# Optimization experiments

Hardware: AMD Instinct MI355X
Metric: run time of the kernel (lower is better)

Reference implementation:

```python
import jax, jax.numpy as jnp
import numpy as np

B, C, H, W = 4, 256, 64, 64
CI = 128  # inter_channels = in_channels // 2
EPS = 1e-5  # torch BatchNorm default eps


def setup_inputs() -> dict:
    key = jax.random.key(0)
    ks = jax.random.split(key, 8)

    def w(k, shape, s=0.02):
        return jax.random.normal(k, shape, jnp.float32) * s

    return {
        "x": jax.random.normal(ks[0], (B, C, H, W), jnp.float32),
        # theta (Q) linear + BatchNorm1d (inference-mode running stats)
        "theta_w": w(ks[1], (CI, C)), "theta_b": jnp.zeros((CI,), jnp.float32),
        "theta_bn_gamma": jnp.ones((CI,), jnp.float32), "theta_bn_beta": jnp.zeros((CI,), jnp.float32),
        "theta_bn_mean": jnp.zeros((CI,), jnp.float32), "theta_bn_var": jnp.ones((CI,), jnp.float32),
        # phi (K) linear + BatchNorm1d
        "phi_w": w(ks[2], (CI, C)), "phi_b": jnp.zeros((CI,), jnp.float32),
        "phi_bn_gamma": jnp.ones((CI,), jnp.float32), "phi_bn_beta": jnp.zeros((CI,), jnp.float32),
        "phi_bn_mean": jnp.zeros((CI,), jnp.float32), "phi_bn_var": jnp.ones((CI,), jnp.float32),
        # g (V) linear
        "g_w": w(ks[3], (CI, C)), "g_b": jnp.zeros((CI,), jnp.float32),
        # W_z output linear
        "wz_w": w(ks[4], (C, CI)), "wz_b": jnp.zeros((C,), jnp.float32),
        # output BatchNorm2d (gamma nonzero instead of init-0 so output is non-trivial)
        "bn_gamma": w(ks[5], (C,), 0.1), "bn_beta": jnp.zeros((C,), jnp.float32),
        "bn_mean": jnp.zeros((C,), jnp.float32), "bn_var": jnp.ones((C,), jnp.float32),
    }


def _linear(z, w, b):
    # z: [B, N, C], w: [D, C] -> [B, N, D]
    return jnp.einsum('bnc,dc->bnd', z, w) + b


def _bn(z, gamma, beta, mean, var):
    # per-channel affine BN in inference mode, channel on last axis
    return (z - mean) * jax.lax.rsqrt(var + EPS) * gamma + beta


def reference(x, theta_w, theta_b, theta_bn_gamma, theta_bn_beta, theta_bn_mean, theta_bn_var,
              phi_w, phi_b, phi_bn_gamma, phi_bn_beta, phi_bn_mean, phi_bn_var,
              g_w, g_b, wz_w, wz_b, bn_gamma, bn_beta, bn_mean, bn_var):
    b, c, h, w = x.shape
    n = h * w
    ci = theta_w.shape[0]
    scale = float(ci) ** (-0.5)

    x_flat = x.reshape(b, c, n).transpose(0, 2, 1)  # [B, N, C]
    Q = _bn(_linear(x_flat, theta_w, theta_b), theta_bn_gamma, theta_bn_beta, theta_bn_mean, theta_bn_var)
    K = _bn(_linear(x_flat, phi_w, phi_b), phi_bn_gamma, phi_bn_beta, phi_bn_mean, phi_bn_var)
    V = _linear(x_flat, g_w, g_b)  # [B, N, CI]

    # attention computed in fp32 (matches torch amp-disabled block)
    attn = jnp.einsum('bnd,bmd->bnm', Q.astype(jnp.float32), K.astype(jnp.float32)) * scale
    attn = jax.nn.softmax(attn, axis=-1).astype(V.dtype)  # [B, N, N]

    y = jnp.einsum('bnm,bmd->bnd', attn, V)  # [B, N, CI]
    y = jnp.einsum('bnd,cd->bnc', y, wz_w) + wz_b  # [B, N, C]
    y = y.transpose(0, 2, 1).reshape(b, c, h, w)

    # BatchNorm2d (inference mode), channel axis 1
    rstd = jax.lax.rsqrt(bn_var + EPS)
    y = (y - bn_mean[None, :, None, None]) * (rstd * bn_gamma)[None, :, None, None] + bn_beta[None, :, None, None]
    return y + x
```

## Files before the change

### kernel.cpp

```cpp
#include <hip/hip_runtime.h>
#include <stdint.h>

typedef __attribute__((ext_vector_type(8))) short bf16x8;
typedef __attribute__((ext_vector_type(4))) float f32x4;

#define WS_WQKV   0u
#define WS_WZ     196608u
#define WS_SCL    262144u
#define WS_SHF    263680u
#define WS_WZS    265216u
#define WS_WZT    266240u
#define WS_Q      524288u
#define WS_K      (WS_Q  + 4194304u)
#define WS_VT     (WS_K  + 4194304u)
#define WS_Y      (WS_VT + 4194304u)
#define WS_OP     (WS_Y  + 4194304u)
#define WS_LP     (WS_OP + 16777216u)

__device__ __forceinline__ short f2bf(float f) {
  union { float f; uint32_t u; } v; v.f = f;
  uint32_t r = v.u + 0x7fffu + ((v.u >> 16) & 1u);
  return (short)(r >> 16);
}

__device__ __forceinline__ f32x4 mfma16(bf16x8 a, bf16x8 b, f32x4 c) {
  return __builtin_amdgcn_mfma_f32_16x16x32_bf16(a, b, c, 0, 0, 0);
}

__global__ __launch_bounds__(256) void prep_kernel(
    const float* theta_w, const float* phi_w, const float* g_w, const float* wz_w,
    const float* theta_b, const float* tg, const float* tb, const float* tm, const float* tv,
    const float* phi_b,   const float* pg, const float* pb, const float* pm, const float* pv,
    const float* g_b,
    const float* wz_b, const float* bg, const float* bb, const float* bm, const float* bv,
    char* ws) {
  int idx = blockIdx.x * 256 + threadIdx.x;
  short* wqkv = (short*)(ws + WS_WQKV);
  if (idx < 98304) {
    float w;
    if (idx < 32768) w = theta_w[idx];
    else if (idx < 65536) w = phi_w[idx - 32768];
    else w = g_w[idx - 65536];
    wqkv[idx] = f2bf(w);
  }
  if (idx < 32768) ((short*)(ws + WS_WZ))[idx] = f2bf(wz_w[idx]);
  if (idx < 384) {
    float s, t;
    if (idx < 128)      { s = tg[idx] * rsqrtf(tv[idx] + 1e-5f);
                          t = (theta_b[idx] - tm[idx]) * s + tb[idx]; }
    else if (idx < 256) { int d = idx - 128; s = pg[d] * rsqrtf(pv[d] + 1e-5f);
                          t = (phi_b[d] - pm[d]) * s + pb[d]; }
    else                { int d = idx - 256; s = 1.0f; t = g_b[d]; }
    ((float*)(ws + WS_SCL))[idx] = s;
    ((float*)(ws + WS_SHF))[idx] = t;
  }
  if (idx < 256) {
    float s = bg[idx] * rsqrtf(bv[idx] + 1e-5f);
    float t = (wz_b[idx] - bm[idx]) * s + bb[idx];
    ((float*)(ws + WS_WZS))[idx] = s;
    ((float*)(ws + WS_WZT))[idx] = t;
  }
}

__global__ __launch_bounds__(256) void qkv_kernel(const float* __restrict__ x, char* ws) {
  const int nt2 = blockIdx.x, b = blockIdx.y;
  const int t = threadIdx.x;
  __shared__ __attribute__((aligned(16))) short xs[32][264];
  const short* wqkv = (const short*)(ws + WS_WQKV);
  const float* scl = (const float*)(ws + WS_SCL);
  const float* shf = (const float*)(ws + WS_SHF);
  const int n0 = nt2 * 32;
  #pragma unroll
  for (int i = 0; i < 8; ++i) {
    int chunk = i * 256 + t;
    int c = chunk >> 3, n4 = chunk & 7;
    const float4 v = *(const float4*)(x + ((size_t)(b * 256 + c) << 12) + n0 + n4 * 4);
    xs[n4 * 4 + 0][c] = f2bf(v.x);
    xs[n4 * 4 + 1][c] = f2bf(v.y);
    xs[n4 * 4 + 2][c] = f2bf(v.z);
    xs[n4 * 4 + 3][c] = f2bf(v.w);
  }
  __syncthreads();
  const int wv = t >> 6, l = t & 63, lr = l & 15, q = l >> 4;
  const int wn = wv & 1, dh = wv >> 1;
  bf16x8 a[8];
  #pragma unroll
  for (int kt = 0; kt < 8; ++kt) a[kt] = *(const bf16x8*)&xs[wn * 16 + lr][kt * 32 + q * 8];
  f32x4 acc[12] = {};
  #pragma unroll
  for (int kt = 0; kt < 8; ++kt) {
    #pragma unroll
    for (int s = 0; s < 12; ++s) {
      const short* wp = wqkv + (size_t)(dh * 192 + s * 16 + lr) * 256 + kt * 32 + q * 8;
      bf16x8 bf = *(const bf16x8*)wp;
      acc[s] = mfma16(a[kt], bf, acc[s]);
    }
  }
  #pragma unroll
  for (int s = 0; s < 12; ++s) {
    int dg = dh * 192 + s * 16 + lr;
    float sc = scl[dg], sh = shf[dg];
    short vals[4];
    #pragma unroll
    for (int r = 0; r < 4; ++r) vals[r] = f2bf(acc[s][r] * sc + sh);
    int nbase = n0 + wn * 16 + q * 4;
    if (dg < 128) {
      short* Q = (short*)(ws + WS_Q) + ((size_t)b << 19);
      #pragma unroll
      for (int r = 0; r < 4; ++r) Q[(size_t)(nbase + r) * 128 + dg] = vals[r];
    } else if (dg < 256) {
      short* K = (short*)(ws + WS_K) + ((size_t)b << 19);
      int d = dg - 128;
      #pragma unroll
      for (int r = 0; r < 4; ++r) K[(size_t)(nbase + r) * 128 + d] = vals[r];
    } else {
      short* VT = (short*)(ws + WS_VT) + ((size_t)b << 19);
      int d = dg - 256;
      short4 pk; pk.x = vals[0]; pk.y = vals[1]; pk.z = vals[2]; pk.w = vals[3];
      *(short4*)(VT + ((size_t)d << 12) + nbase) = pk;
    }
  }
}

__global__ __launch_bounds__(256, 3) void attn_kernel(char* ws) {
  const int g = blockIdx.x;
  const int b = (g & 7) >> 1;
  const int idx = ((g >> 3) << 1) | (g & 1);
  const int nt = idx >> 2, mc = idx & 3;
  const int t = threadIdx.x, wv = t >> 6, l = t & 63, lr = l & 15, q = l >> 4;
  __shared__ __attribute__((aligned(16))) short ks[64][136];
  __shared__ __attribute__((aligned(16))) short vs[128][72];
  __shared__ __attribute__((aligned(16))) short ps[4][16][72];
  const short* Q  = (const short*)(ws + WS_Q)  + ((size_t)b << 19);
  const short* K  = (const short*)(ws + WS_K)  + ((size_t)b << 19);
  const short* VT = (const short*)(ws + WS_VT) + ((size_t)b << 19);
  const int n0w = nt * 64 + wv * 16;
  bf16x8 qf[4];
  {
    const short* qp = Q + (size_t)(n0w + lr) * 128 + q * 8;
    #pragma unroll
    for (int kt = 0; kt < 4; ++kt) qf[kt] = *(const bf16x8*)(qp + kt * 32);
  }
  f32x4 o[8] = {};
  float lsum[4] = {0.f, 0.f, 0.f, 0.f};
  const float s2 = 0.08838834764831845f * 1.4426950408889634f;
  const int mbase = mc << 10;

  for (int it = 0; it < 16; ++it) {
    const int m0 = mbase + it * 64;
    __syncthreads();
    #pragma unroll
    for (int i = 0; i < 4; ++i) {
      int chunk = i * 256 + t;
      int row = chunk >> 4, dq = chunk & 15;
      *(uint4*)&ks[row][dq * 8] = *(const uint4*)(K + (size_t)(m0 + row) * 128 + dq * 8);
    }
    #pragma unroll
    for (int i = 0; i < 4; ++i) {
      int chunk = i * 256 + t;
      int row = chunk >> 3, mq = chunk & 7;
      *(uint4*)&vs[row][mq * 8] = *(const uint4*)(VT + ((size_t)row << 12) + m0 + mq * 8);
    }
    __syncthreads();
    f32x4 sacc[4] = {};
    #pragma unroll
    for (int kt = 0; kt < 4; ++kt) {
      #pragma unroll
      for (int s = 0; s < 4; ++s) {
        bf16x8 kf = *(const bf16x8*)&ks[s * 16 + lr][kt * 32 + q * 8];
        sacc[s] = mfma16(qf[kt], kf, sacc[s]);
      }
    }
    float pvv[4][4];
    #pragma unroll
    for (int s = 0; s < 4; ++s)
      #pragma unroll
      for (int r = 0; r < 4; ++r)
        pvv[s][r] = exp2f(sacc[s][r] * s2);
    #pragma unroll
    for (int r = 0; r < 4; ++r)
      lsum[r] += (pvv[0][r] + pvv[1][r]) + (pvv[2][r] + pvv[3][r]);
    #pragma unroll
    for (int s = 0; s < 4; ++s)
      #pragma unroll
      for (int r = 0; r < 4; ++r)
        ps[wv][q * 4 + r][s * 16 + lr] = f2bf(pvv[s][r]);
    bf16x8 pf0 = *(const bf16x8*)&ps[wv][lr][q * 8];
    bf16x8 pf1 = *(const bf16x8*)&ps[wv][lr][32 + q * 8];
    #pragma unroll
    for (int dt = 0; dt < 8; ++dt) {
      bf16x8 vf0 = *(const bf16x8*)&vs[dt * 16 + lr][q * 8];
      o[dt] = mfma16(pf0, vf0, o[dt]);
      bf16x8 vf1 = *(const bf16x8*)&vs[dt * 16 + lr][32 + q * 8];
      o[dt] = mfma16(pf1, vf1, o[dt]);
    }
  }
  const int cb = mc * 4 + b;
  float* LP = (float*)(ws + WS_LP) + ((size_t)cb << 12);
  #pragma unroll
  for (int r = 0; r < 4; ++r) {
    float s = lsum[r];
    s += __shfl_xor(s, 1, 64);
    s += __shfl_xor(s, 2, 64);
    s += __shfl_xor(s, 4, 64);
    s += __shfl_xor(s, 8, 64);
    if (lr == 0) LP[n0w + q * 4 + r] = s;
  }
  short* OPc = (short*)(ws + WS_OP) + ((size_t)cb << 19);
  #pragma unroll
  for (int dt = 0; dt < 8; ++dt)
    #pragma unroll
    for (int r = 0; r < 4; ++r)
      OPc[((size_t)(n0w + q * 4 + r) << 7) + dt * 16 + lr] = f2bf(o[dt][r]);
}

__global__ __launch_bounds__(256) void proj_kernel(const float* __restrict__ x,
                                                   char* ws, float* __restrict__ out) {
  const int nt = blockIdx.x, b = blockIdx.y;
  const int t = threadIdx.x, wv = t >> 6, l = t & 63, lr = l & 15, q = l >> 4;
  __shared__ __attribute__((aligned(16))) short ys[16][136];
  const short* OP = (const short*)(ws + WS_OP);
  const float* LP = (const float*)(ws + WS_LP);
  const short* WZ = (const short*)(ws + WS_WZ);
  const float* wzs = (const float*)(ws + WS_WZS);
  const float* wzt = (const float*)(ws + WS_WZT);
  const int n0 = nt * 16;
  {
    int row = t >> 4, d8 = (t & 15) * 8;
    int n = n0 + row;
    float acc8[8] = {};
    float lsf = 0.f;
    #pragma unroll
    for (int mc = 0; mc < 4; ++mc) {
      int cb = mc * 4 + b;
      const short* p = OP + ((size_t)cb << 19) + ((size_t)n << 7) + d8;
      uint4 v = *(const uint4*)p;
      uint32_t uu[4] = {v.x, v.y, v.z, v.w};
      #pragma unroll
      for (int w = 0; w < 4; ++w) {
        union { uint32_t u; float f; } lo, hi;
        lo.u = uu[w] << 16; hi.u = uu[w] & 0xffff0000u;
        acc8[w * 2 + 0] += lo.f;
        acc8[w * 2 + 1] += hi.f;
      }
      lsf += LP[(cb << 12) + n];
    }
    float inv = 1.0f / lsf;
    short out8[8];
    #pragma unroll
    for (int j = 0; j < 8; ++j) out8[j] = f2bf(acc8[j] * inv);
    *(uint4*)&ys[row][d8] = *(uint4*)out8;
  }
  __syncthreads();
  bf16x8 a[4];
  #pragma unroll
  for (int kt = 0; kt < 4; ++kt) a[kt] = *(const bf16x8*)&ys[lr][kt * 32 + q * 8];
  f32x4 acc[4] = {};
  #pragma unroll
  for (int kt = 0; kt < 4; ++kt) {
    #pragma unroll
    for (int s = 0; s < 4; ++s) {
      const short* wp = WZ + (size_t)(wv * 64 + s * 16 + lr) * 128 + kt * 32 + q * 8;
      bf16x8 bf = *(const bf16x8*)wp;
      acc[s] = mfma16(a[kt], bf, acc[s]);
    }
  }
  #pragma unroll
  for (int s = 0; s < 4; ++s) {
    int c = wv * 64 + s * 16 + lr;
    float sc = wzs[c], sh = wzt[c];
    int nbase = n0 + q * 4;
    size_t base = ((size_t)(b * 256 + c) << 12) + nbase;
    float4 xv = *(const float4*)(x + base);
    float4 ov;
    ov.x = acc[s][0] * sc + sh + xv.x;
    ov.y = acc[s][1] * sc + sh + xv.y;
    ov.z = acc[s][2] * sc + sh + xv.z;
    ov.w = acc[s][3] * sc + sh + xv.w;
    *(float4*)(out + base) = ov;
  }
}

extern "C" void kernel_launch(void* const* d_in, const int* in_sizes, int n_in,
                              void* d_out, int out_size, void* d_ws, size_t ws_size,
                              hipStream_t stream) {
  const float* x       = (const float*)d_in[0];
  const float* theta_w = (const float*)d_in[1];
  const float* theta_b = (const float*)d_in[2];
  const float* tg      = (const float*)d_in[3];
  const float* tb      = (const float*)d_in[4];
  const float* tm      = (const float*)d_in[5];
  const float* tv      = (const float*)d_in[6];
  const float* phi_w   = (const float*)d_in[7];
  const float* phi_b   = (const float*)d_in[8];
  const float* pg      = (const float*)d_in[9];
  const float* pb      = (const float*)d_in[10];
  const float* pm      = (const float*)d_in[11];
  const float* pv      = (const float*)d_in[12];
  const float* g_w     = (const float*)d_in[13];
  const float* g_b     = (const float*)d_in[14];
  const float* wz_w    = (const float*)d_in[15];
  const float* wz_b    = (const float*)d_in[16];
  const float* bg      = (const float*)d_in[17];
  const float* bb      = (const float*)d_in[18];
  const float* bm      = (const float*)d_in[19];
  const float* bv      = (const float*)d_in[20];
  char* ws = (char*)d_ws;
  float* out = (float*)d_out;

  prep_kernel<<<384, 256, 0, stream>>>(theta_w, phi_w, g_w, wz_w,
                                       theta_b, tg, tb, tm, tv,
                                       phi_b, pg, pb, pm, pv,
                                       g_b, wz_b, bg, bb, bm, bv, ws);
  qkv_kernel<<<dim3(128, 4), 256, 0, stream>>>(x, ws);
  attn_kernel<<<1024, 256, 0, stream>>>(ws);
  proj_kernel<<<dim3(256, 4), 256, 0, stream>>>(x, ws, out);
}
```

Before: 216.5 us.

## Read K/V fragments straight from global memory and give each wave 32 query rows

The attention kernel no longer stages K and V^T tiles in shared memory behind two __syncthreads per iteration. Each lane now loads its MFMA fragments directly from global memory, relying on the caches. Each wave handles two 16-row query groups, so every K/V fragment feeds two MFMAs, and the grid is halved to 512 blocks with the occupancy hint lowered to 2. This removes LDS traffic and block-level synchronisation, but exposes global-load latency with no explicit prefetch and raises register pressure.

```diff
diff --git a/kernel.cpp b/kernel.cpp
--- a/kernel.cpp
+++ b/kernel.cpp
@@ -122,96 +122,97 @@
   }
 }
 
-__global__ __launch_bounds__(256, 3) void attn_kernel(char* ws) {
+__global__ __launch_bounds__(256, 2) void attn_kernel(char* ws) {
   const int g = blockIdx.x;
   const int b = (g & 7) >> 1;
   const int idx = ((g >> 3) << 1) | (g & 1);
   const int nt = idx >> 2, mc = idx & 3;
   const int t = threadIdx.x, wv = t >> 6, l = t & 63, lr = l & 15, q = l >> 4;
-  __shared__ __attribute__((aligned(16))) short ks[64][136];
-  __shared__ __attribute__((aligned(16))) short vs[128][72];
-  __shared__ __attribute__((aligned(16))) short ps[4][16][72];
+  __shared__ __attribute__((aligned(16))) short ps[4][32][72];
   const short* Q  = (const short*)(ws + WS_Q)  + ((size_t)b << 19);
   const short* K  = (const short*)(ws + WS_K)  + ((size_t)b << 19);
   const short* VT = (const short*)(ws + WS_VT) + ((size_t)b << 19);
-  const int n0w = nt * 64 + wv * 16;
-  bf16x8 qf[4];
-  {
-    const short* qp = Q + (size_t)(n0w + lr) * 128 + q * 8;
-    #pragma unroll
-    for (int kt = 0; kt < 4; ++kt) qf[kt] = *(const bf16x8*)(qp + kt * 32);
-  }
-  f32x4 o[8] = {};
-  float lsum[4] = {0.f, 0.f, 0.f, 0.f};
+  const int n0w = nt * 128 + wv * 32;
+  bf16x8 qf[2][4];
+  #pragma unroll
+  for (int j = 0; j < 2; ++j) {
+    const short* qp = Q + (size_t)(n0w + j * 16 + lr) * 128 + q * 8;
+    #pragma unroll
+    for (int kt = 0; kt < 4; ++kt) qf[j][kt] = *(const bf16x8*)(qp + kt * 32);
+  }
+  f32x4 o[2][8] = {};
+  float lsum[2][4] = {};
   const float s2 = 0.08838834764831845f * 1.4426950408889634f;
   const int mbase = mc << 10;
 
   for (int it = 0; it < 16; ++it) {
     const int m0 = mbase + it * 64;
-    __syncthreads();
-    #pragma unroll
-    for (int i = 0; i < 4; ++i) {
-      int chunk = i * 256 + t;
-      int row = chunk >> 4, dq = chunk & 15;
-      *(uint4*)&ks[row][dq * 8] = *(const uint4*)(K + (size_t)(m0 + row) * 128 + dq * 8);
-    }
-    #pragma unroll
-    for (int i = 0; i < 4; ++i) {
-      int chunk = i * 256 + t;
-      int row = chunk >> 3, mq = chunk & 7;
-      *(uint4*)&vs[row][mq * 8] = *(const uint4*)(VT + ((size_t)row << 12) + m0 + mq * 8);
-    }
-    __syncthreads();
-    f32x4 sacc[4] = {};
+    f32x4 sacc[2][4] = {};
+    const short* kp = K + ((size_t)(m0 + lr) << 7) + q * 8;
     #pragma unroll
     for (int kt = 0; kt < 4; ++kt) {
       #pragma unroll
       for (int s = 0; s < 4; ++s) {
-        bf16x8 kf = *(const bf16x8*)&ks[s * 16 + lr][kt * 32 + q * 8];
-        sacc[s] = mfma16(qf[kt], kf, sacc[s]);
+        bf16x8 kf = *(const bf16x8*)(kp + (s << 11) + kt * 32);
+        sacc[0][s] = mfma16(qf[0][kt], kf, sacc[0][s]);
+        sacc[1][s] = mfma16(qf[1][kt], kf, sacc[1][s]);
       }
     }
-    float pvv[4][4];
-    #pragma unroll
-    for (int s = 0; s < 4; ++s)
+    #pragma unroll
+    for (int j = 0; j < 2; ++j) {
+      float pvv[4][4];
+      #pragma unroll
+      for (int s = 0; s < 4; ++s)
+        #pragma unroll
+        for (int r = 0; r < 4; ++r)
+          pvv[s][r] = exp2f(sacc[j][s][r] * s2);
       #pragma unroll
       for (int r = 0; r < 4; ++r)
-        pvv[s][r] = exp2f(sacc[s][r] * s2);
-    #pragma unroll
-    for (int r = 0; r < 4; ++r)
-      lsum[r] += (pvv[0][r] + pvv[1][r]) + (pvv[2][r] + pvv[3][r]);
-    #pragma unroll
-    for (int s = 0; s < 4; ++s)
-      #pragma unroll
-      for (int r = 0; r < 4; ++r)
-        ps[wv][q * 4 + r][s * 16 + lr] = f2bf(pvv[s][r]);
-    bf16x8 pf0 = *(const bf16x8*)&ps[wv][lr][q * 8];
-    bf16x8 pf1 = *(const bf16x8*)&ps[wv][lr][32 + q * 8];
+        lsum[j][r] += (pvv[0][r] + pvv[1][r]) + (pvv[2][r] + pvv[3][r]);
+      #pragma unroll
+      for (int s = 0; s < 4; ++s)
+        #pragma unroll
+        for (int r = 0; r < 4; ++r)
+          ps[wv][j * 16 + q * 4 + r][s * 16 + lr] = f2bf(pvv[s][r]);
+    }
+    bf16x8 pf[2][2];
+    #pragma unroll
+    for (int j = 0; j < 2; ++j)
+      #pragma unroll
+      for (int h = 0; h < 2; ++h)
+        pf[j][h] = *(const bf16x8*)&ps[wv][j * 16 + lr][h * 32 + q * 8];
+    const short* vp = VT + ((size_t)lr << 12) + m0 + q * 8;
     #pragma unroll
     for (int dt = 0; dt < 8; ++dt) {
-      bf16x8 vf0 = *(const bf16x8*)&vs[dt * 16 + lr][q * 8];
-      o[dt] = mfma16(pf0, vf0, o[dt]);
-      bf16x8 vf1 = *(const bf16x8*)&vs[dt * 16 + lr][32 + q * 8];
-      o[dt] = mfma16(pf1, vf1, o[dt]);
+      #pragma unroll
+      for (int h = 0; h < 2; ++h) {
+        bf16x8 vf = *(const bf16x8*)(vp + ((size_t)dt << 16) + h * 32);
+        o[0][dt] = mfma16(pf[0][h], vf, o[0][dt]);
+        o[1][dt] = mfma16(pf[1][h], vf, o[1][dt]);
+      }
     }
   }
   const int cb = mc * 4 + b;
   float* LP = (float*)(ws + WS_LP) + ((size_t)cb << 12);
   #pragma unroll
-  for (int r = 0; r < 4; ++r) {
-    float s = lsum[r];
-    s += __shfl_xor(s, 1, 64);
-    s += __shfl_xor(s, 2, 64);
-    s += __shfl_xor(s, 4, 64);
-    s += __shfl_xor(s, 8, 64);
-    if (lr == 0) LP[n0w + q * 4 + r] = s;
-  }
+  for (int j = 0; j < 2; ++j)
+    #pragma unroll
+    for (int r = 0; r < 4; ++r) {
+      float s = lsum[j][r];
+      s += __shfl_xor(s, 1, 64);
+      s += __shfl_xor(s, 2, 64);
+      s += __shfl_xor(s, 4, 64);
+      s += __shfl_xor(s, 8, 64);
+      if (lr == 0) LP[n0w + j * 16 + q * 4 + r] = s;
+    }
   short* OPc = (short*)(ws + WS_OP) + ((size_t)cb << 19);
   #pragma unroll
-  for (int dt = 0; dt < 8; ++dt)
-    #pragma unroll
-    for (int r = 0; r < 4; ++r)
-      OPc[((size_t)(n0w + q * 4 + r) << 7) + dt * 16 + lr] = f2bf(o[dt][r]);
+  for (int j = 0; j < 2; ++j)
+    #pragma unroll
+    for (int dt = 0; dt < 8; ++dt)
+      #pragma unroll
+      for (int r = 0; r < 4; ++r)
+        OPc[((size_t)(n0w + j * 16 + q * 4 + r) << 7) + dt * 16 + lr] = f2bf(o[j][dt][r]);
 }
 
 __global__ __launch_bounds__(256) void proj_kernel(const float* __restrict__ x,
@@ -313,6 +314,6 @@
                                        phi_b, pg, pb, pm, pv,
                                        g_b, wz_b, bg, bb, bm, bv, ws);
   qkv_kernel<<<dim3(128, 4), 256, 0, stream>>>(x, ws);
-  attn_kernel<<<1024, 256, 0, stream>>>(ws);
+  attn_kernel<<<512, 256, 0, stream>>>(ws);
   proj_kernel<<<dim3(256, 4), 256, 0, stream>>>(x, ws, out);
 }
```

Result: slower. 295.7 us (+36.6%).
